# Performance work log

Measured on AMD Instinct MI355X. Metric: run time of the kernel, lower is better.

The kernel has to match this reference:

```python
import jax, jax.numpy as jnp
import numpy as np

SEG_LENS = [2048, 8192]
DIL_RATES = [1, 2]


def _dilated_attention(q, k, v, is_causal):
    # q,k,v: [b, n, h, d]
    b, n, h, d = q.shape
    ng = len(SEG_LENS)
    g = h // ng  # heads per group (even split)
    scale = 1.0 / np.sqrt(d).astype(np.float32)
    out = jnp.zeros_like(q)
    for i, (s, r) in enumerate(zip(SEG_LENS, DIL_RATES)):
        hs = i * g
        offset = i % r  # offset_idx % dilation_rate, as in _create_dilation_pattern
        idx = np.arange(offset, s, r)  # dilated positions within a segment, length m
        m = idx.shape[0]
        ns = n // s  # number of segments
        # reshape to segments then gather dilated positions: [b, ns, m, g, d]
        qg = q[:, :, hs:hs + g, :].reshape(b, ns, s, g, d)[:, :, idx]
        kg = k[:, :, hs:hs + g, :].reshape(b, ns, s, g, d)[:, :, idx]
        vg = v[:, :, hs:hs + g, :].reshape(b, ns, s, g, d)[:, :, idx]
        # segment-local attention over dilated tokens only (structured sparsity)
        scores = jnp.einsum('bsqhd,bskhd->bshqk', qg, kg) * scale
        if is_causal:
            cm = np.tril(np.ones((m, m), dtype=bool))  # idx is sorted -> causal in dilated order
            scores = jnp.where(cm, scores, -jnp.inf)
        attn = jax.nn.softmax(scores, axis=-1)
        og = jnp.einsum('bshqk,bskhd->bsqhd', attn, vg)  # [b, ns, m, g, d]
        # scatter back to full segment positions; non-dilated positions stay zero
        full = jnp.zeros((b, ns, s, g, d), q.dtype).at[:, :, idx].set(og)
        out = out.at[:, :, hs:hs + g, :].set(full.reshape(b, n, g, d))
    return out


def setup_inputs() -> dict:
    key = jax.random.key(0)
    k1, k2, k3 = jax.random.split(key, 3)
    shape = (1, 8192, 8, 64)
    q = jax.random.normal(k1, shape, dtype=jnp.float32)
    k = jax.random.normal(k2, shape, dtype=jnp.float32)
    v = jax.random.normal(k3, shape, dtype=jnp.float32)
    return {"q": q, "k": k, "v": v, "is_causal": 1}


def reference(q, k, v, is_causal):
    return _dilated_attention(q, k, v, bool(is_causal))
```

## Files before the change

kernel.cpp:

```cpp
#include <hip/hip_runtime.h>


#define LP 72

typedef __attribute__((ext_vector_type(8))) short bf16x8;
typedef __attribute__((ext_vector_type(4))) float f32x4;
typedef const unsigned int __attribute__((address_space(1)))* gp1;
typedef unsigned int __attribute__((address_space(3)))* lp3;

__device__ __forceinline__ unsigned short f2bf(float f) {
  unsigned u = __builtin_bit_cast(unsigned, f);
  u += 0x7fff + ((u >> 16) & 1);
  return (unsigned short)(u >> 16);
}

__device__ __forceinline__ int region_base(int head) {
  return (head < 4) ? head * 524288 : 2097152 + (head - 4) * 262144;
}

__device__ __forceinline__ void gl_lds16(const unsigned short* g, unsigned short* l) {
  __builtin_amdgcn_global_load_lds((gp1)g, (lp3)l, 16, 0, 0);
}

__global__ __launch_bounds__(256, 4)
void prep_kernel(const float* __restrict__ K, const float* __restrict__ V,
                 unsigned short* __restrict__ Kb, unsigned short* __restrict__ Vt) {
  __shared__ unsigned short sT[64][LP];
  const int bid = blockIdx.x;
  int head, pos0, rate, off;
  if (bid < 512) { head = bid >> 7; pos0 = (bid & 127) * 64; rate = 1; off = 0; }
  else { int b = bid - 512; head = 4 + (b >> 6); pos0 = (b & 63) * 64; rate = 2; off = 1; }
  const int rb = region_base(head);
  const int tid = threadIdx.x;
  const int row = tid >> 2, dg = tid & 3;
  const long tok = (long)(pos0 + row) * rate + off;

  {
    const float* kp = K + tok * 512 + head * 64 + dg * 16;
    unsigned short tmp[16];
    #pragma unroll
    for (int i = 0; i < 4; ++i) {
      float4 f = ((const float4*)kp)[i];
      tmp[i * 4 + 0] = f2bf(f.x); tmp[i * 4 + 1] = f2bf(f.y);
      tmp[i * 4 + 2] = f2bf(f.z); tmp[i * 4 + 3] = f2bf(f.w);
    }
    const int s = row & 7;
    unsigned short* dstrow = Kb + rb + (long)(pos0 + row) * 64;
    *(int4*)(dstrow + (((2 * dg)     ^ s) * 8)) = ((int4*)tmp)[0];
    *(int4*)(dstrow + (((2 * dg + 1) ^ s) * 8)) = ((int4*)tmp)[1];
  }

  {
    const float* vp = V + tok * 512 + head * 64 + dg * 16;
    #pragma unroll
    for (int i = 0; i < 4; ++i) {
      float4 f = ((const float4*)vp)[i];
      unsigned* p = (unsigned*)&sT[row][dg * 16 + i * 4];
      p[0] = (unsigned)f2bf(f.x) | ((unsigned)f2bf(f.y) << 16);
      p[1] = (unsigned)f2bf(f.z) | ((unsigned)f2bf(f.w) << 16);
    }
  }
  __syncthreads();

  {
    const int wv = tid >> 6, lane = tid & 63;
    unsigned pk[8];
    #pragma unroll
    for (int j = 0; j < 8; ++j) {
      unsigned lo = sT[wv * 16 + 2 * j][lane];
      unsigned hi = sT[wv * 16 + 2 * j + 1][lane];
      pk[j] = lo | (hi << 16);
    }
    const int s = lane & 7;
    unsigned short* dstrow = Vt + rb + (long)pos0 * 64 + lane * 64;
    int4 a = {(int)pk[0], (int)pk[1], (int)pk[2], (int)pk[3]};
    int4 b = {(int)pk[4], (int)pk[5], (int)pk[6], (int)pk[7]};
    *(int4*)(dstrow + (((2 * wv)     ^ s) * 8)) = a;
    *(int4*)(dstrow + (((2 * wv + 1) ^ s) * 8)) = b;
  }
}

__global__ __launch_bounds__(256, 2)
void attn_kernel(const float* __restrict__ Q, const unsigned short* __restrict__ Kb,
                 const unsigned short* __restrict__ Vt, const int* __restrict__ IC,
                 float* __restrict__ O, float* __restrict__ Slots) {
  __shared__ __attribute__((aligned(16))) unsigned short sK[2][4096];
  __shared__ __attribute__((aligned(16))) unsigned short sV[2][4096];
  __shared__ __attribute__((aligned(16))) unsigned short sP[4][1024];

  const int bid = blockIdx.x;
  int head, q0, seg0, mseg, rate, off, grp, chunk, slot;
  if (bid < 512) {
    int t = 63 - (bid >> 3);
    int h4 = (bid >> 1) & 3;
    head = 4 + h4; seg0 = 0; mseg = 4096;
    rate = 2; off = 1; grp = 1;
    q0 = t * 64;
    chunk = bid & 1;
    slot = (h4 * 64 + t) * 2 + chunk;
  } else {
    int cc = bid - 512;
    int t = cc >> 4;
    int job = cc & 15;
    head = job & 3;
    seg0 = (job >> 2) * 2048;
    q0 = seg0 + t * 64; mseg = 2048;
    rate = 1; off = 0; grp = 0; chunk = 0; slot = 0;
  }
  const int rb = region_base(head);
  const bool causal = (*IC) != 0;
  const int tid = threadIdx.x, wave = tid >> 6, lane = tid & 63;
  const int l16 = lane & 15, quad = lane >> 4;
  const int ch0 = ((quad ^ (l16 & 7)) * 8);
  const int ch1 = ch0 ^ 32;

  const int qloc = q0 - seg0;
  const int diagkb = qloc >> 6;
  const int nkb = causal ? diagkb + 1 : (mseg >> 6);
  const int klo = grp ? chunk * 32 : 0;
  const int khi = grp ? min(nkb, klo + 32) : nkb;
  if (klo >= khi) return;

  const float QSCALE = 0.18033688011112042f;
  bf16x8 aQ[2];
  {
    long tok = (long)(q0 + wave * 16 + l16) * rate + off;
    const float* qp = Q + tok * 512 + head * 64 + quad * 8;
    #pragma unroll
    for (int kc = 0; kc < 2; ++kc) {
      float4 f0 = ((const float4*)(qp + kc * 32))[0];
      float4 f1 = ((const float4*)(qp + kc * 32))[1];
      bf16x8 a;
      a[0] = (short)f2bf(f0.x * QSCALE); a[1] = (short)f2bf(f0.y * QSCALE);
      a[2] = (short)f2bf(f0.z * QSCALE); a[3] = (short)f2bf(f0.w * QSCALE);
      a[4] = (short)f2bf(f1.x * QSCALE); a[5] = (short)f2bf(f1.y * QSCALE);
      a[6] = (short)f2bf(f1.z * QSCALE); a[7] = (short)f2bf(f1.w * QSCALE);
      aQ[kc] = a;
    }
  }

  f32x4 oacc[4], lacc;
  lacc = (f32x4){0.f, 0.f, 0.f, 0.f};
  #pragma unroll
  for (int dt = 0; dt < 4; ++dt) oacc[dt] = (f32x4){0.f, 0.f, 0.f, 0.f};
  bf16x8 vones;
  #pragma unroll
  for (int i = 0; i < 8; ++i) vones[i] = (short)0x3F80;

  unsigned short* myP = &sP[wave][0];
  const unsigned short* Ksrc = Kb + rb + (long)seg0 * 64;
  const unsigned short* Vsrc = Vt + rb + (long)seg0 * 64;

  const int o0 = wave * 1024;
  const int lo = lane * 8;
  {
    const unsigned short* kt = Ksrc + (long)klo * 4096;
    const unsigned short* vt = Vsrc + (long)klo * 4096;
    gl_lds16(kt + o0 + lo,       &sK[0][o0]);
    gl_lds16(kt + o0 + 512 + lo, &sK[0][o0 + 512]);
    gl_lds16(vt + o0 + lo,       &sV[0][o0]);
    gl_lds16(vt + o0 + 512 + lo, &sV[0][o0 + 512]);
  }

  for (int kb = klo; kb < khi; ++kb) {
    const int cur = (kb - klo) & 1;
    __syncthreads();
    if (kb + 1 < khi) {
      const unsigned short* kt = Ksrc + (long)(kb + 1) * 4096;
      const unsigned short* vt = Vsrc + (long)(kb + 1) * 4096;
      gl_lds16(kt + o0 + lo,       &sK[cur ^ 1][o0]);
      gl_lds16(kt + o0 + 512 + lo, &sK[cur ^ 1][o0 + 512]);
      gl_lds16(vt + o0 + lo,       &sV[cur ^ 1][o0]);
      gl_lds16(vt + o0 + 512 + lo, &sV[cur ^ 1][o0 + 512]);
    }
    const unsigned short* kbuf = &sK[cur][0];
    const unsigned short* vbuf = &sV[cur][0];

    f32x4 sc[4];
    #pragma unroll
    for (int c = 0; c < 4; ++c) {
      const unsigned short* krow = &kbuf[(c * 16 + l16) * 64];
      bf16x8 b0 = *(const bf16x8*)(krow + ch0);
      bf16x8 b1 = *(const bf16x8*)(krow + ch1);
      f32x4 z = (f32x4){0.f, 0.f, 0.f, 0.f};
      z = __builtin_amdgcn_mfma_f32_16x16x32_bf16(aQ[0], b0, z, 0, 0, 0);
      z = __builtin_amdgcn_mfma_f32_16x16x32_bf16(aQ[1], b1, z, 0, 0, 0);
      sc[c] = z;
    }

    const bool needMask = causal && (kb == diagkb);
    #pragma unroll
    for (int c = 0; c < 4; ++c) {
      #pragma unroll
      for (int r = 0; r < 4; ++r) {
        float e = __builtin_amdgcn_exp2f(sc[c][r]);
        if (needMask && (kb * 64 + c * 16 + l16 > qloc + wave * 16 + quad * 4 + r)) e = 0.f;
        const int qrow = quad * 4 + r;
        const int cidx = c * 2 + (l16 >> 3);
        myP[qrow * 64 + ((cidx ^ (qrow & 7)) << 3) + (l16 & 7)] = f2bf(e);
      }
    }
    const int swr = l16 & 7;
    bf16x8 aP0 = *(const bf16x8*)&myP[l16 * 64 + ((quad ^ swr) << 3)];
    bf16x8 aP1 = *(const bf16x8*)&myP[l16 * 64 + (((quad + 4) ^ swr) << 3)];
    lacc = __builtin_amdgcn_mfma_f32_16x16x32_bf16(aP0, vones, lacc, 0, 0, 0);
    lacc = __builtin_amdgcn_mfma_f32_16x16x32_bf16(aP1, vones, lacc, 0, 0, 0);

    #pragma unroll
    for (int dt = 0; dt < 4; ++dt) {
      const unsigned short* vrow = &vbuf[(dt * 16 + l16) * 64];
      bf16x8 v0 = *(const bf16x8*)(vrow + ch0);
      bf16x8 v1 = *(const bf16x8*)(vrow + ch1);
      oacc[dt] = __builtin_amdgcn_mfma_f32_16x16x32_bf16(aP0, v0, oacc[dt], 0, 0, 0);
      oacc[dt] = __builtin_amdgcn_mfma_f32_16x16x32_bf16(aP1, v1, oacc[dt], 0, 0, 0);
    }
  }

  if (grp == 1) {
    float* S = Slots + (long)slot * 4160;
    #pragma unroll
    for (int r = 0; r < 4; ++r) {
      int row = wave * 16 + quad * 4 + r;
      #pragma unroll
      for (int dt = 0; dt < 4; ++dt)
        S[row * 64 + dt * 16 + l16] = oacc[dt][r];
    }
    if (l16 == 0) {
      #pragma unroll
      for (int r = 0; r < 4; ++r)
        S[4096 + wave * 16 + quad * 4 + r] = lacc[r];
    }
  } else {
    #pragma unroll
    for (int r = 0; r < 4; ++r) {
      int tq = q0 + wave * 16 + quad * 4 + r;
      long tok = (long)tq * rate + off;
      float inv = 1.0f / lacc[r];
      float* dst = O + tok * 512 + head * 64 + l16;
      #pragma unroll
      for (int dt = 0; dt < 4; ++dt)
        dst[dt * 16] = oacc[dt][r] * inv;
    }
  }
}

__global__ __launch_bounds__(256, 4)
void combine_kernel(const float* __restrict__ Slots, const int* __restrict__ IC,
                    float* __restrict__ O) {
  const int b = blockIdx.x;
  const int h4 = b >> 6, t = b & 63;
  const bool causal = (*IC) != 0;
  const int nkb = causal ? t + 1 : 64;
  const int nc = (nkb > 32) ? 2 : 1;
  const float* s0 = Slots + (long)((h4 * 64 + t) * 2) * 4160;
  const int tid = threadIdx.x;
  const int row = tid >> 2, dq = (tid & 3) * 16;

  float4 acc[4];
  const float4* p0 = (const float4*)(s0 + row * 64 + dq);
  #pragma unroll
  for (int i = 0; i < 4; ++i) acc[i] = p0[i];
  float l = s0[4096 + row];
  if (nc == 2) {
    const float* s1 = s0 + 4160;
    const float4* p1 = (const float4*)(s1 + row * 64 + dq);
    #pragma unroll
    for (int i = 0; i < 4; ++i) {
      float4 v = p1[i];
      acc[i].x += v.x; acc[i].y += v.y; acc[i].z += v.z; acc[i].w += v.w;
    }
    l += s1[4096 + row];
  }
  const float inv = 1.0f / l;
  const long tok = (long)(t * 64 + row) * 2 + 1;
  float* dst = O + tok * 512 + (4 + h4) * 64 + dq;
  #pragma unroll
  for (int i = 0; i < 4; ++i) {
    float4 o = {acc[i].x * inv, acc[i].y * inv, acc[i].z * inv, acc[i].w * inv};
    ((float4*)dst)[i] = o;
  }
  float* dste = O + (tok - 1) * 512 + (4 + h4) * 64 + dq;
  const float4 z = {0.f, 0.f, 0.f, 0.f};
  #pragma unroll
  for (int i = 0; i < 4; ++i) ((float4*)dste)[i] = z;
}

extern "C" void kernel_launch(void* const* d_in, const int* in_sizes, int n_in,
                              void* d_out, int out_size, void* d_ws, size_t ws_size,
                              hipStream_t stream) {
  const float* q = (const float*)d_in[0];
  const float* k = (const float*)d_in[1];
  const float* v = (const float*)d_in[2];
  const int* ic = (const int*)d_in[3];
  unsigned short* Kb = (unsigned short*)d_ws;
  unsigned short* Vt = Kb + 3145728;
  float* Slots = (float*)((char*)d_ws + 12582912);
  prep_kernel<<<dim3(768), dim3(256), 0, stream>>>(k, v, Kb, Vt);
  attn_kernel<<<dim3(1024), dim3(256), 0, stream>>>(q, Kb, Vt, ic, (float*)d_out, Slots);
  combine_kernel<<<dim3(256), dim3(256), 0, stream>>>(Slots, ic, (float*)d_out);
}
```

Baseline: 144.3 us.

## Fuse split-K combine into attention kernel via atomic counters, transpose MFMA operands

Removes the separate combine kernel. The last-arriving chunk of each split tile now merges partial outputs through a global atomic counter, and tiles with a single chunk write the final output directly. The MFMA operands are swapped so each lane holds one query row, which lets the row sum be computed with scalar adds and two shuffles instead of an extra ones-vector MFMA, and lets outputs be written as float4. This saves a kernel launch and extra MFMAs, at the cost of threadfences, an atomic, and counter zeroing added to the prep kernel.

```diff
diff --git a/kernel.cpp b/kernel.cpp
--- a/kernel.cpp
+++ b/kernel.cpp
@@ -24,14 +24,16 @@
 
 __global__ __launch_bounds__(256, 4)
 void prep_kernel(const float* __restrict__ K, const float* __restrict__ V,
-                 unsigned short* __restrict__ Kb, unsigned short* __restrict__ Vt) {
+                 unsigned short* __restrict__ Kb, unsigned short* __restrict__ Vt,
+                 int* __restrict__ Cnt) {
   __shared__ unsigned short sT[64][LP];
   const int bid = blockIdx.x;
+  const int tid = threadIdx.x;
+  if (bid == 0 && tid < 256) Cnt[tid] = 0;
   int head, pos0, rate, off;
   if (bid < 512) { head = bid >> 7; pos0 = (bid & 127) * 64; rate = 1; off = 0; }
   else { int b = bid - 512; head = 4 + (b >> 6); pos0 = (b & 63) * 64; rate = 2; off = 1; }
   const int rb = region_base(head);
-  const int tid = threadIdx.x;
   const int row = tid >> 2, dg = tid & 3;
   const long tok = (long)(pos0 + row) * rate + off;
 
@@ -83,13 +85,13 @@
 __global__ __launch_bounds__(256, 2)
 void attn_kernel(const float* __restrict__ Q, const unsigned short* __restrict__ Kb,
                  const unsigned short* __restrict__ Vt, const int* __restrict__ IC,
-                 float* __restrict__ O, float* __restrict__ Slots) {
+                 float* __restrict__ O, float* __restrict__ Slots, int* __restrict__ Cnt) {
   __shared__ __attribute__((aligned(16))) unsigned short sK[2][4096];
   __shared__ __attribute__((aligned(16))) unsigned short sV[2][4096];
   __shared__ __attribute__((aligned(16))) unsigned short sP[4][1024];
 
   const int bid = blockIdx.x;
-  int head, q0, seg0, mseg, rate, off, grp, chunk, slot;
+  int head, q0, seg0, mseg, rate, off, grp, chunk, tile;
   if (bid < 512) {
     int t = 63 - (bid >> 3);
     int h4 = (bid >> 1) & 3;
@@ -97,7 +99,7 @@
     rate = 2; off = 1; grp = 1;
     q0 = t * 64;
     chunk = bid & 1;
-    slot = (h4 * 64 + t) * 2 + chunk;
+    tile = h4 * 64 + t;
   } else {
     int cc = bid - 512;
     int t = cc >> 4;
@@ -105,7 +107,7 @@
     head = job & 3;
     seg0 = (job >> 2) * 2048;
     q0 = seg0 + t * 64; mseg = 2048;
-    rate = 1; off = 0; grp = 0; chunk = 0; slot = 0;
+    rate = 1; off = 0; grp = 0; chunk = 0; tile = 0;
   }
   const int rb = region_base(head);
   const bool causal = (*IC) != 0;
@@ -120,9 +122,10 @@
   const int klo = grp ? chunk * 32 : 0;
   const int khi = grp ? min(nkb, klo + 32) : nkb;
   if (klo >= khi) return;
+  const int nc = (grp && nkb > 32) ? 2 : 1;
 
   const float QSCALE = 0.18033688011112042f;
-  bf16x8 aQ[2];
+  bf16x8 bQ[2];
   {
     long tok = (long)(q0 + wave * 16 + l16) * rate + off;
     const float* qp = Q + tok * 512 + head * 64 + quad * 8;
@@ -135,17 +138,14 @@
       a[2] = (short)f2bf(f0.z * QSCALE); a[3] = (short)f2bf(f0.w * QSCALE);
       a[4] = (short)f2bf(f1.x * QSCALE); a[5] = (short)f2bf(f1.y * QSCALE);
       a[6] = (short)f2bf(f1.z * QSCALE); a[7] = (short)f2bf(f1.w * QSCALE);
-      aQ[kc] = a;
-    }
-  }
-
-  f32x4 oacc[4], lacc;
-  lacc = (f32x4){0.f, 0.f, 0.f, 0.f};
+      bQ[kc] = a;
+    }
+  }
+
+  f32x4 oacc[4];
+  float lsum = 0.f;
   #pragma unroll
   for (int dt = 0; dt < 4; ++dt) oacc[dt] = (f32x4){0.f, 0.f, 0.f, 0.f};
-  bf16x8 vones;
-  #pragma unroll
-  for (int i = 0; i < 8; ++i) vones[i] = (short)0x3F80;
 
   unsigned short* myP = &sP[wave][0];
   const unsigned short* Ksrc = Kb + rb + (long)seg0 * 64;
@@ -180,109 +180,99 @@
     #pragma unroll
     for (int c = 0; c < 4; ++c) {
       const unsigned short* krow = &kbuf[(c * 16 + l16) * 64];
-      bf16x8 b0 = *(const bf16x8*)(krow + ch0);
-      bf16x8 b1 = *(const bf16x8*)(krow + ch1);
+      bf16x8 a0 = *(const bf16x8*)(krow + ch0);
+      bf16x8 a1 = *(const bf16x8*)(krow + ch1);
       f32x4 z = (f32x4){0.f, 0.f, 0.f, 0.f};
-      z = __builtin_amdgcn_mfma_f32_16x16x32_bf16(aQ[0], b0, z, 0, 0, 0);
-      z = __builtin_amdgcn_mfma_f32_16x16x32_bf16(aQ[1], b1, z, 0, 0, 0);
+      z = __builtin_amdgcn_mfma_f32_16x16x32_bf16(a0, bQ[0], z, 0, 0, 0);
+      z = __builtin_amdgcn_mfma_f32_16x16x32_bf16(a1, bQ[1], z, 0, 0, 0);
       sc[c] = z;
     }
 
     const bool needMask = causal && (kb == diagkb);
+    const int myq = qloc + wave * 16 + l16;
+    const int sw = l16 & 7;
     #pragma unroll
     for (int c = 0; c < 4; ++c) {
+      unsigned short pb[4];
       #pragma unroll
       for (int r = 0; r < 4; ++r) {
         float e = __builtin_amdgcn_exp2f(sc[c][r]);
-        if (needMask && (kb * 64 + c * 16 + l16 > qloc + wave * 16 + quad * 4 + r)) e = 0.f;
-        const int qrow = quad * 4 + r;
-        const int cidx = c * 2 + (l16 >> 3);
-        myP[qrow * 64 + ((cidx ^ (qrow & 7)) << 3) + (l16 & 7)] = f2bf(e);
+        if (needMask && (kb * 64 + c * 16 + quad * 4 + r > myq)) e = 0.f;
+        lsum += e;
+        pb[r] = f2bf(e);
       }
-    }
-    const int swr = l16 & 7;
-    bf16x8 aP0 = *(const bf16x8*)&myP[l16 * 64 + ((quad ^ swr) << 3)];
-    bf16x8 aP1 = *(const bf16x8*)&myP[l16 * 64 + (((quad + 4) ^ swr) << 3)];
-    lacc = __builtin_amdgcn_mfma_f32_16x16x32_bf16(aP0, vones, lacc, 0, 0, 0);
-    lacc = __builtin_amdgcn_mfma_f32_16x16x32_bf16(aP1, vones, lacc, 0, 0, 0);
+      unsigned w0 = (unsigned)pb[0] | ((unsigned)pb[1] << 16);
+      unsigned w1 = (unsigned)pb[2] | ((unsigned)pb[3] << 16);
+      const int wch = (c * 2 + (quad >> 1)) ^ sw;
+      uint2* dst = (uint2*)&myP[l16 * 64 + wch * 8 + (quad & 1) * 4];
+      *dst = (uint2){w0, w1};
+    }
+    bf16x8 bP0 = *(const bf16x8*)&myP[l16 * 64 + (((0 * 4 + quad) ^ sw) * 8)];
+    bf16x8 bP1 = *(const bf16x8*)&myP[l16 * 64 + (((1 * 4 + quad) ^ sw) * 8)];
 
     #pragma unroll
     for (int dt = 0; dt < 4; ++dt) {
       const unsigned short* vrow = &vbuf[(dt * 16 + l16) * 64];
       bf16x8 v0 = *(const bf16x8*)(vrow + ch0);
       bf16x8 v1 = *(const bf16x8*)(vrow + ch1);
-      oacc[dt] = __builtin_amdgcn_mfma_f32_16x16x32_bf16(aP0, v0, oacc[dt], 0, 0, 0);
-      oacc[dt] = __builtin_amdgcn_mfma_f32_16x16x32_bf16(aP1, v1, oacc[dt], 0, 0, 0);
-    }
-  }
-
-  if (grp == 1) {
+      oacc[dt] = __builtin_amdgcn_mfma_f32_16x16x32_bf16(v0, bP0, oacc[dt], 0, 0, 0);
+      oacc[dt] = __builtin_amdgcn_mfma_f32_16x16x32_bf16(v1, bP1, oacc[dt], 0, 0, 0);
+    }
+  }
+
+  lsum += __shfl_xor(lsum, 16);
+  lsum += __shfl_xor(lsum, 32);
+
+  const int row = wave * 16 + l16;
+
+  if (nc == 1) {
+    long tok = (long)(q0 + row) * rate + off;
+    float inv = 1.0f / lsum;
+    float* dst = O + tok * 512 + head * 64 + quad * 4;
+    #pragma unroll
+    for (int dt = 0; dt < 4; ++dt) {
+      float4 v = {oacc[dt][0] * inv, oacc[dt][1] * inv, oacc[dt][2] * inv, oacc[dt][3] * inv};
+      *(float4*)(dst + dt * 16) = v;
+    }
+    if (grp == 1) {
+      int p = q0 + (tid >> 2);
+      float4 z4 = {0.f, 0.f, 0.f, 0.f};
+      float4* dste = (float4*)(O + (long)(2 * p) * 512 + head * 64 + (tid & 3) * 16);
+      dste[0] = z4; dste[1] = z4; dste[2] = z4; dste[3] = z4;
+    }
+  } else {
+    const int slot = tile * 2 + chunk;
     float* S = Slots + (long)slot * 4160;
     #pragma unroll
-    for (int r = 0; r < 4; ++r) {
-      int row = wave * 16 + quad * 4 + r;
+    for (int dt = 0; dt < 4; ++dt)
+      *(float4*)&S[row * 64 + dt * 16 + quad * 4] =
+          (float4){oacc[dt][0], oacc[dt][1], oacc[dt][2], oacc[dt][3]};
+    if (quad == 0) S[4096 + row] = lsum;
+    __threadfence();
+    __syncthreads();
+    volatile int* flag = (volatile int*)&sP[0][0];
+    if (tid == 0) *(int*)flag = atomicAdd(&Cnt[tile], 1);
+    __syncthreads();
+    if (*flag == 1) {
+      __threadfence();
+      const float* So = Slots + (long)(tile * 2 + (chunk ^ 1)) * 4160;
+      float ltot = lsum + So[4096 + row];
+      float inv = 1.0f / ltot;
+      long tok = (long)(q0 + row) * rate + off;
+      float* dst = O + tok * 512 + head * 64 + quad * 4;
       #pragma unroll
-      for (int dt = 0; dt < 4; ++dt)
-        S[row * 64 + dt * 16 + l16] = oacc[dt][r];
-    }
-    if (l16 == 0) {
-      #pragma unroll
-      for (int r = 0; r < 4; ++r)
-        S[4096 + wave * 16 + quad * 4 + r] = lacc[r];
-    }
-  } else {
-    #pragma unroll
-    for (int r = 0; r < 4; ++r) {
-      int tq = q0 + wave * 16 + quad * 4 + r;
-      long tok = (long)tq * rate + off;
-      float inv = 1.0f / lacc[r];
-      float* dst = O + tok * 512 + head * 64 + l16;
-      #pragma unroll
-      for (int dt = 0; dt < 4; ++dt)
-        dst[dt * 16] = oacc[dt][r] * inv;
-    }
-  }
-}
-
-__global__ __launch_bounds__(256, 4)
-void combine_kernel(const float* __restrict__ Slots, const int* __restrict__ IC,
-                    float* __restrict__ O) {
-  const int b = blockIdx.x;
-  const int h4 = b >> 6, t = b & 63;
-  const bool causal = (*IC) != 0;
-  const int nkb = causal ? t + 1 : 64;
-  const int nc = (nkb > 32) ? 2 : 1;
-  const float* s0 = Slots + (long)((h4 * 64 + t) * 2) * 4160;
-  const int tid = threadIdx.x;
-  const int row = tid >> 2, dq = (tid & 3) * 16;
-
-  float4 acc[4];
-  const float4* p0 = (const float4*)(s0 + row * 64 + dq);
-  #pragma unroll
-  for (int i = 0; i < 4; ++i) acc[i] = p0[i];
-  float l = s0[4096 + row];
-  if (nc == 2) {
-    const float* s1 = s0 + 4160;
-    const float4* p1 = (const float4*)(s1 + row * 64 + dq);
-    #pragma unroll
-    for (int i = 0; i < 4; ++i) {
-      float4 v = p1[i];
-      acc[i].x += v.x; acc[i].y += v.y; acc[i].z += v.z; acc[i].w += v.w;
-    }
-    l += s1[4096 + row];
-  }
-  const float inv = 1.0f / l;
-  const long tok = (long)(t * 64 + row) * 2 + 1;
-  float* dst = O + tok * 512 + (4 + h4) * 64 + dq;
-  #pragma unroll
-  for (int i = 0; i < 4; ++i) {
-    float4 o = {acc[i].x * inv, acc[i].y * inv, acc[i].z * inv, acc[i].w * inv};
-    ((float4*)dst)[i] = o;
-  }
-  float* dste = O + (tok - 1) * 512 + (4 + h4) * 64 + dq;
-  const float4 z = {0.f, 0.f, 0.f, 0.f};
-  #pragma unroll
-  for (int i = 0; i < 4; ++i) ((float4*)dste)[i] = z;
+      for (int dt = 0; dt < 4; ++dt) {
+        float4 v = *(const float4*)&So[row * 64 + dt * 16 + quad * 4];
+        float4 o = {(oacc[dt][0] + v.x) * inv, (oacc[dt][1] + v.y) * inv,
+                    (oacc[dt][2] + v.z) * inv, (oacc[dt][3] + v.w) * inv};
+        *(float4*)(dst + dt * 16) = o;
+      }
+      int p = q0 + (tid >> 2);
+      float4 z4 = {0.f, 0.f, 0.f, 0.f};
+      float4* dste = (float4*)(O + (long)(2 * p) * 512 + head * 64 + (tid & 3) * 16);
+      dste[0] = z4; dste[1] = z4; dste[2] = z4; dste[3] = z4;
+    }
+  }
 }
 
 extern "C" void kernel_launch(void* const* d_in, const int* in_sizes, int n_in,
@@ -295,7 +285,7 @@
   unsigned short* Kb = (unsigned short*)d_ws;
   unsigned short* Vt = Kb + 3145728;
   float* Slots = (float*)((char*)d_ws + 12582912);
-  prep_kernel<<<dim3(768), dim3(256), 0, stream>>>(k, v, Kb, Vt);
-  attn_kernel<<<dim3(1024), dim3(256), 0, stream>>>(q, Kb, Vt, ic, (float*)d_out, Slots);
-  combine_kernel<<<dim3(256), dim3(256), 0, stream>>>(Slots, ic, (float*)d_out);
-}
+  int* Cnt = (int*)((char*)d_ws + 12582912 + 8519680);
+  prep_kernel<<<dim3(768), dim3(256), 0, stream>>>(k, v, Kb, Vt, Cnt);
+  attn_kernel<<<dim3(1024), dim3(256), 0, stream>>>(q, Kb, Vt, ic, (float*)d_out, Slots, Cnt);
+}
```

Result: slower. 191.5 us (+32.7%).
